# Kernel optimization log

Measured on AMD Instinct MI355X. Metric: run time of the kernel, lower is better.

Reference implementation:

```python
import jax, jax.numpy as jnp
import numpy as np

B, L, D, H = 4, 2048, 256, 512


def silu_backward(x):
    s = jax.nn.silu(x)
    return s + jax.nn.sigmoid(x) * (1.0 - s)


def setup_inputs() -> dict:
    key = jax.random.key(0)
    ks = jax.random.split(key, 12)
    sc = 0.02
    return {
        "x": jax.random.normal(ks[0], (B, L, D), jnp.float32),
        "W1": jax.random.normal(ks[1], (B, H, D), jnp.float32) * sc,
        "W2": jax.random.normal(ks[2], (B, D, H), jnp.float32) * sc,
        "Wq": jax.random.normal(ks[3], (D, D), jnp.float32) * sc,
        "bq": jnp.zeros((D,), jnp.float32),
        "Wk": jax.random.normal(ks[4], (D, D), jnp.float32) * sc,
        "bk": jnp.zeros((D,), jnp.float32),
        "Wv": jax.random.normal(ks[5], (D, D), jnp.float32) * sc,
        "bv": jnp.zeros((D,), jnp.float32),
        "w_lr": jax.random.normal(ks[6], (D,), jnp.float32) * sc,
        "b_lr": jnp.zeros((), jnp.float32),
        "w_wd": jax.random.normal(ks[7], (D,), jnp.float32) * sc,
        "b_wd": jnp.zeros((), jnp.float32),
        "log_base_lr": jnp.asarray(np.log(0.1), jnp.float32),
        "log_base_wd": jnp.asarray(np.log(0.5), jnp.float32),
    }


def reference(x, W1, W2, Wq, bq, Wk, bk, Wv, bv, w_lr, b_lr, w_wd, b_wd, log_base_lr, log_base_wd):
    b, l, d = x.shape
    query = x @ Wq + bq
    key = x @ Wk + bk
    value = x @ Wv + bv
    lr = jnp.exp(log_base_lr) * jax.nn.sigmoid(x @ w_lr + b_lr)          # [b,l]
    log_wd = jnp.log(1.0 - jnp.exp(log_base_wd) * jax.nn.sigmoid(x @ w_wd + b_wd))  # [b,l]

    wd_cross = jnp.exp(jnp.cumsum(log_wd, axis=1))                       # [b,l]
    idx = jnp.arange(l)
    strict_upper = idx[:, None] < idx[None, :]                           # (m, j): j > m
    A = jnp.where(strict_upper[None], log_wd[:, None, :], 0.0)           # [b,m,j]
    wd_inner = jnp.exp(jnp.cumsum(A, axis=2)) * (idx[:, None] <= idx[None, :])[None]  # [b,m,j]

    X1 = key
    Z1 = jnp.einsum('bhd,bld->blh', W1, X1)
    X2 = jax.nn.silu(Z1)
    Z2 = jnp.einsum('bdh,blh->bld', W2, X2)
    grad_Z2 = Z2 - value
    grad_X2 = jnp.einsum('bdh,bld->blh', W2, grad_Z2)
    grad_Z1 = silu_backward(Z1) * grad_X2

    X1_ = query
    mask_X1X1_ = jnp.einsum('bld,bmd->blm', X1, X1_) * wd_inner
    Z1_inner = -jnp.einsum('blh,bl,blm->bmh', grad_Z1, lr, mask_X1X1_)
    Z1_cross = jnp.einsum('bhd,bld,bl->blh', W1, X1_, wd_cross)
    Z1_ = Z1_inner + Z1_cross

    W1_next = (-jnp.einsum('blh,bl,bld->bhd', grad_Z1, lr * wd_inner[:, :, -1], X1)
               + W1 * wd_cross[:, -1][:, None, None])

    X2_ = jax.nn.silu(Z1_)
    mask_X2X2_ = jnp.einsum('blh,bmh->blm', X2, X2_) * wd_inner
    Z2_inner = -jnp.einsum('bld,bl,blm->bmd', grad_Z2, lr, mask_X2X2_)
    Z2_cross = jnp.einsum('bdh,blh,bl->bld', W2, X2_, wd_cross)
    Z2_ = Z2_inner + Z2_cross

    W2_next = (-jnp.einsum('bld,bl,blh->bdh', grad_Z2, lr * wd_inner[:, :, -1], X2)
               + W2 * wd_cross[:, -1][:, None, None])

    return (Z2_, W1_next, W2_next)
```

## Files before the change

kernel.cpp:

```cpp
#include <hip/hip_runtime.h>

typedef __bf16 bf16;
typedef __bf16 bf16x8 __attribute__((ext_vector_type(8)));
typedef __bf16 bf16x4 __attribute__((ext_vector_type(4)));
typedef float  f32x4  __attribute__((ext_vector_type(4)));

#define SB 72
#define CUTOFF -18.0

__device__ __forceinline__ float silu_f(float x){
  float s = 1.f/(1.f+__expf(-x));
  return x*s;
}
__device__ __forceinline__ float silu_bwd_f(float x){
  float s = 1.f/(1.f+__expf(-x));
  float si = x*s;
  return si + s*(1.f-si);
}

struct MArgs {
  const bf16* A; const bf16* B;
  long sA, sB;
  int lda, ldb;
  int M, N, K;
  int mode;
  float* Cf; long sCf;
  bf16*  Cb; long sCb;
  bf16*  Cb2; long sCb2;
  bf16*  Ct;  long sCt;  int ldct;
  int ldc;
  const float* auxf; int ldax; long sAuxf;
  const bf16*  auxb; long sAuxb;
  const float* rowv; long sRowv;
  const double* cd;  long sCd;
  const float* ks;   long sKs;
  const float* clp;  long sClp;
  bf16* Q; bf16* Ko; float* Vo; const float* bqkv;
};

template<int TM>
__device__ __forceinline__ void gemm_body(const MArgs& g, int bm, int bn, int bz)
{
  const int row0 = bm*TM, col0 = bn*64;
  constexpr int NI  = TM/32;
  constexpr int TPR = 256/TM;
  constexpr int EPR = 64/TPR;
  constexpr int NCH = EPR/8;

  const bf16* A = g.A + (long)bz*g.sA;
  const bf16* B = g.B + (long)bz*g.sB;
  const float* ksp = g.ks ? g.ks + (long)bz*g.sKs : (const float*)0;
  const double* cd = g.cd ? g.cd + (long)bz*g.sCd : (const double*)0;
  float* Cf = g.Cf ? g.Cf + (long)bz*g.sCf : (float*)0;
  bf16* Cb  = g.Cb ? g.Cb + (long)bz*g.sCb : (bf16*)0;
  bf16* Cb2 = g.Cb2 ? g.Cb2 + (long)bz*g.sCb2 : (bf16*)0;
  bf16* Ct  = g.Ct ? g.Ct + (long)bz*g.sCt : (bf16*)0;
  const float* auxf = g.auxf ? g.auxf + (long)bz*g.sAuxf : (const float*)0;
  const bf16*  auxb = g.auxb ? g.auxb + (long)bz*g.sAuxb : (const bf16*)0;
  const float* rowv = g.rowv ? g.rowv + (long)bz*g.sRowv : (const float*)0;

  const int tid = threadIdx.x;
  const int mode = g.mode;
  const int lane = tid & 63;
  const int w = tid >> 6;
  const int wr = (w >> 1) * (TM/2), wc = (w & 1) * 32;
  const int l15 = lane & 15;
  const int quad = lane >> 4;

  __shared__ __align__(16) bf16 As[TM*SB];
  __shared__ __align__(16) bf16 Bs[64*SB];

  f32x4 acc[NI][2];
  #pragma unroll
  for (int i=0;i<NI;i++)
    #pragma unroll
    for (int j=0;j<2;j++)
      #pragma unroll
      for (int r=0;r<4;r++) acc[i][j][r] = 0.f;

  const int rowA = tid / TPR, kA = (tid % TPR) * EPR;
  const int rowB = tid >> 2,  kB = (tid & 3) * 16;

  int klo = 0;
  if (cd && ksp) {
    const double cref = cd[g.K-1];
    while (klo + 64 < g.K && (cref - cd[klo+63]) < CUTOFF) klo += 64;
  }

  for (int k0 = klo; k0 < g.K; k0 += 64) {
    {
      const bf16* s = A + (long)(row0+rowA)*g.lda + k0 + kA;
      bf16x8 v[NCH];
      #pragma unroll
      for (int p=0;p<NCH;p++) v[p] = *(const bf16x8*)(s + p*8);
      if (ksp) {
        #pragma unroll
        for (int p=0;p<NCH;p++)
          #pragma unroll
          for (int i=0;i<8;i++)
            v[p][i] = (bf16)((float)v[p][i] * ksp[k0+kA+p*8+i]);
      }
      #pragma unroll
      for (int p=0;p<NCH;p++) *(bf16x8*)&As[rowA*SB + kA + p*8] = v[p];
    }
    {
      const bf16* s = B + (long)(col0+rowB)*g.ldb + k0 + kB;
      *(bf16x8*)&Bs[rowB*SB + kB]     = *(const bf16x8*)s;
      *(bf16x8*)&Bs[rowB*SB + kB + 8] = *(const bf16x8*)(s+8);
    }
    __syncthreads();
    #pragma unroll
    for (int ch=0; ch<2; ch++){
      bf16x8 af[NI], bf2[2];
      #pragma unroll
      for (int i=0;i<NI;i++) af[i]  = *(const bf16x8*)&As[(wr + i*16 + l15)*SB + ch*32 + quad*8];
      #pragma unroll
      for (int j=0;j<2;j++) bf2[j] = *(const bf16x8*)&Bs[(wc + j*16 + l15)*SB + ch*32 + quad*8];
      #pragma unroll
      for (int i=0;i<NI;i++)
        #pragma unroll
        for (int j=0;j<2;j++)
          acc[i][j] = __builtin_amdgcn_mfma_f32_16x16x32_bf16(af[i], bf2[j], acc[i][j], 0, 0, 0);
    }
    __syncthreads();
  }

  float clv = 0.f;
  if (mode == 10) clv = *(g.clp + (long)bz*g.sClp);

  #pragma unroll
  for (int i=0;i<NI;i++){
    const int rb = row0 + wr + i*16 + quad*4;
    #pragma unroll
    for (int j=0;j<2;j++){
      const int c = col0 + wc + j*16 + l15;
      bf16 tv[4]; bool doT = false;
      #pragma unroll
      for (int reg=0; reg<4; reg++){
        const int r = rb + reg;
        float v = acc[i][j][reg];
        const long co = (long)r*g.ldc + c;
        switch (mode) {
          case 1: {
            Cb[co]  = (bf16)v;
            bf16 sv = (bf16)silu_f(v);
            Cb2[co] = sv;
            tv[reg] = sv; doT = true;
          } break;
          case 2: {
            bf16 o = (bf16)(v - auxf[(long)r*g.ldax + c]);
            Cb[co] = o; tv[reg] = o; doT = true;
          } break;
          case 3: {
            bf16 o = (bf16)(silu_bwd_f((float)auxb[(long)r*g.ldax + c]) * v * rowv[r]);
            Cb[co] = o; tv[reg] = o; doT = true;
          } break;
          case 10: {
            Cf[co] = v + auxf[(long)r*g.ldax + c]*clv;
          } break;
          case 11: {
            float o = v + g.bqkv[c];
            if (c < 256)      g.Q [(long)r*256 + c]       = (bf16)o;
            else if (c < 512) { g.Ko[(long)r*256 + (c-256)] = (bf16)o; tv[reg] = (bf16)o; doT = true; }
            else              g.Vo[(long)r*256 + (c-512)] = o;
          } break;
        }
      }
      if (doT && Ct) {
        bf16x4 t4 = { tv[0], tv[1], tv[2], tv[3] };
        if (mode == 11) {
          const int b = rb / g.ldct, l = rb % g.ldct;
          *(bf16x4*)&Ct[(long)b*g.sCt + (long)(c-256)*g.ldct + l] = t4;
        } else {
          *(bf16x4*)&Ct[(long)c*g.ldct + rb] = t4;
        }
      }
    }
  }
}

__global__ __launch_bounds__(256)
void mfma_gemm128(MArgs g){ gemm_body<128>(g, blockIdx.x, blockIdx.y, blockIdx.z); }

__global__ __launch_bounds__(256)
void mfma_gemm64(MArgs g){ gemm_body<64>(g, blockIdx.x, blockIdx.y, blockIdx.z); }

__global__ __launch_bounds__(256)
void wnext_gemm(MArgs g1, MArgs g2){
  const int z = blockIdx.z;
  const MArgs& g = (z < 4) ? g1 : g2;
  const int bz = z & 3;
  if ((int)blockIdx.x*128 >= g.M || (int)blockIdx.y*64 >= g.N) return;
  gemm_body<128>(g, blockIdx.x, blockIdx.y, bz);
}

struct PArgs {
  const bf16 *A, *B1;
  long sA, sB1;
  const double* cd; long sCd;
  const float* lrv; long sLr;
  bf16* P;
};

template<int KS64, int ISLR>
__global__ __launch_bounds__(256)
void pgen(PArgs g)
{
  const int mt = blockIdx.x, slot = blockIdx.y, bz = blockIdx.z;
  const int m0 = mt*64;
  const int l0 = (m0 & ~127) - slot*128;
  if (l0 < 0) return;
  const double* cd = g.cd + (long)bz*g.sCd;
  const int lref = (l0+127 < m0) ? (l0+127) : m0;
  if (cd[m0] - cd[lref] < CUTOFF) return;

  const int K1 = KS64*64;
  const bf16* A  = g.A  + (long)bz*g.sA;
  const bf16* B1 = g.B1 + (long)bz*g.sB1;
  const float* lrv = ISLR ? (g.lrv + (long)bz*g.sLr) : (const float*)0;

  const int tid = threadIdx.x;
  const int lane = tid & 63, w = tid >> 6;
  const int wr = (w>>1)*32, wc = (w&1)*64;
  const int l15 = lane & 15, quad = lane >> 4;
  const int rowA = tid >> 2, kA = (tid & 3) * 16;
  const int rowB = tid >> 1, kB = (tid & 1) * 32;

  __shared__ __align__(16) bf16 As[64*SB];
  __shared__ __align__(16) bf16 Bs[128*SB];

  f32x4 O[2][4];
  #pragma unroll
  for (int i=0;i<2;i++)
    #pragma unroll
    for (int j=0;j<4;j++)
      #pragma unroll
      for (int r=0;r<4;r++) O[i][j][r] = 0.f;

  for (int ks=0; ks<KS64; ks++){
    const int k0 = ks*64;
    {
      const bf16* s = A + (long)(m0+rowA)*K1 + k0 + kA;
      *(bf16x8*)&As[rowA*SB + kA]     = *(const bf16x8*)s;
      *(bf16x8*)&As[rowA*SB + kA + 8] = *(const bf16x8*)(s+8);
    }
    {
      const bf16* s = B1 + (long)(l0+rowB)*K1 + k0 + kB;
      #pragma unroll
      for (int p=0;p<4;p++) *(bf16x8*)&Bs[rowB*SB + kB + p*8] = *(const bf16x8*)(s + p*8);
    }
    __syncthreads();
    #pragma unroll
    for (int ch=0; ch<2; ch++){
      bf16x8 af[2], bfr[4];
      #pragma unroll
      for (int i=0;i<2;i++) af[i]  = *(const bf16x8*)&As[(wr + i*16 + l15)*SB + ch*32 + quad*8];
      #pragma unroll
      for (int j=0;j<4;j++) bfr[j] = *(const bf16x8*)&Bs[(wc + j*16 + l15)*SB + ch*32 + quad*8];
      #pragma unroll
      for (int i=0;i<2;i++)
        #pragma unroll
        for (int j=0;j<4;j++)
          O[i][j] = __builtin_amdgcn_mfma_f32_16x16x32_bf16(af[i], bfr[j], O[i][j], 0, 0, 0);
    }
    __syncthreads();
  }

  bf16* Pt = g.P + (((long)bz*32 + mt)*3 + slot) * (64*128);
  float cl[4], lv[4];
  #pragma unroll
  for (int j=0;j<4;j++){
    const int l = l0 + wc + j*16 + l15;
    cl[j] = (float)cd[l];
    if (ISLR) lv[j] = lrv[l];
  }
  #pragma unroll
  for (int i=0;i<2;i++)
    #pragma unroll
    for (int reg=0; reg<4; reg++){
      const int mloc = wr + i*16 + quad*4 + reg;
      const int m = m0 + mloc;
      const float cm = (float)cd[m];
      #pragma unroll
      for (int j=0;j<4;j++){
        const int lloc = wc + j*16 + l15;
        const int l = l0 + lloc;
        float v = -O[i][j][reg] * __expf(cm - cl[j]);
        if (ISLR) v *= lv[j];
        if (l > m) v = 0.f;
        Pt[mloc*128 + lloc] = (bf16)v;
      }
    }
}

struct CArgs {
  const bf16 *A, *W, *P, *B2;
  long sA, sW, sB2;
  int ldb2;
  const double* cd; long sCd;
  const float* wdc; long sWdc;
  float* Cf; long sCf;
  bf16* Cb; long sCb;
  int ldc;
};

template<int KS64, int SILU, int ZSPLIT>
__global__ __launch_bounds__(256)
void cons(CArgs g)
{
  const int mt = blockIdx.x;
  const int m0 = mt*64, n0 = blockIdx.y*64;
  const int bz   = ZSPLIT ? (blockIdx.z >> 1) : blockIdx.z;
  const int half = ZSPLIT ? (blockIdx.z & 1)  : 0;
  const int K1 = KS64*64;
  const bf16* A  = g.A  + (long)bz*g.sA;
  const bf16* W  = g.W  + (long)bz*g.sW;
  const bf16* B2 = g.B2 + (long)bz*g.sB2;
  const double* cd = g.cd + (long)bz*g.sCd;
  const float* wdc = g.wdc + (long)bz*g.sWdc;

  const int tid = threadIdx.x;
  const int lane = tid & 63, w = tid >> 6;
  const int wr = (w>>1)*32, wc = (w&1)*32;
  const int l15 = lane & 15, quad = lane >> 4;
  const int rowA = tid >> 2, kA = (tid & 3) * 16;

  bool alive[3];
  int nalive = 0;
  #pragma unroll
  for (int s=0;s<3;s++){
    const int l0 = (m0 & ~127) - s*128;
    bool a = (l0 >= 0);
    if (a) {
      const int lref = (l0+127 < m0) ? (l0+127) : m0;
      a = (cd[m0] - cd[lref] >= CUTOFF);
    }
    alive[s] = a; nalive += a ? 1 : 0;
  }
  if (ZSPLIT && half == 1 && nalive == 0) return;

  __shared__ __align__(16) bf16 As[64*SB];
  __shared__ __align__(16) bf16 Bs[64*SB];

  f32x4 O[2][2];
  #pragma unroll
  for (int i=0;i<2;i++)
    #pragma unroll
    for (int j=0;j<2;j++)
      #pragma unroll
      for (int r=0;r<4;r++) O[i][j][r] = 0.f;

  if (half == 0) {
    for (int ks=0; ks<KS64; ks++){
      const int k0 = ks*64;
      {
        const bf16* s = A + (long)(m0+rowA)*K1 + k0 + kA;
        *(bf16x8*)&As[rowA*SB + kA]     = *(const bf16x8*)s;
        *(bf16x8*)&As[rowA*SB + kA + 8] = *(const bf16x8*)(s+8);
      }
      {
        const bf16* s = W + (long)(n0+rowA)*K1 + k0 + kA;
        *(bf16x8*)&Bs[rowA*SB + kA]     = *(const bf16x8*)s;
        *(bf16x8*)&Bs[rowA*SB + kA + 8] = *(const bf16x8*)(s+8);
      }
      __syncthreads();
      #pragma unroll
      for (int ch=0; ch<2; ch++){
        bf16x8 af[2], bfr[2];
        #pragma unroll
        for (int i=0;i<2;i++) af[i]  = *(const bf16x8*)&As[(wr + i*16 + l15)*SB + ch*32 + quad*8];
        #pragma unroll
        for (int j=0;j<2;j++) bfr[j] = *(const bf16x8*)&Bs[(wc + j*16 + l15)*SB + ch*32 + quad*8];
        #pragma unroll
        for (int i=0;i<2;i++)
          #pragma unroll
          for (int j=0;j<2;j++)
            O[i][j] = __builtin_amdgcn_mfma_f32_16x16x32_bf16(af[i], bfr[j], O[i][j], 0, 0, 0);
      }
      __syncthreads();
    }
    #pragma unroll
    for (int i=0;i<2;i++)
      #pragma unroll
      for (int reg=0; reg<4; reg++){
        const float s = wdc[m0 + wr + i*16 + quad*4 + reg];
        #pragma unroll
        for (int j=0;j<2;j++) O[i][j][reg] *= s;
      }
  }

  if (!ZSPLIT || half == 1) {
    for (int s=0; s<3; s++){
      if (!alive[s]) continue;
      const int l0 = (m0 & ~127) - s*128;
      const bf16* Pt = g.P + (((long)bz*32 + mt)*3 + s) * (64*128);
      for (int hk=0; hk<2; hk++){
        {
          const bf16* sp = Pt + (long)rowA*128 + hk*64 + kA;
          *(bf16x8*)&As[rowA*SB + kA]     = *(const bf16x8*)sp;
          *(bf16x8*)&As[rowA*SB + kA + 8] = *(const bf16x8*)(sp+8);
        }
        {
          const bf16* sp = B2 + (long)(n0+rowA)*g.ldb2 + l0 + hk*64 + kA;
          *(bf16x8*)&Bs[rowA*SB + kA]     = *(const bf16x8*)sp;
          *(bf16x8*)&Bs[rowA*SB + kA + 8] = *(const bf16x8*)(sp+8);
        }
        __syncthreads();
        #pragma unroll
        for (int ch=0; ch<2; ch++){
          bf16x8 af[2], bfr[2];
          #pragma unroll
          for (int i=0;i<2;i++) af[i]  = *(const bf16x8*)&As[(wr + i*16 + l15)*SB + ch*32 + quad*8];
          #pragma unroll
          for (int j=0;j<2;j++) bfr[j] = *(const bf16x8*)&Bs[(wc + j*16 + l15)*SB + ch*32 + quad*8];
          #pragma unroll
          for (int i=0;i<2;i++)
            #pragma unroll
            for (int j=0;j<2;j++)
              O[i][j] = __builtin_amdgcn_mfma_f32_16x16x32_bf16(af[i], bfr[j], O[i][j], 0, 0, 0);
        }
        __syncthreads();
      }
    }
  }

  #pragma unroll
  for (int i=0;i<2;i++){
    const int rb = m0 + wr + i*16 + quad*4;
    #pragma unroll
    for (int j=0;j<2;j++){
      const int c = n0 + wc + j*16 + l15;
      #pragma unroll
      for (int reg=0; reg<4; reg++){
        const long co = (long)(rb+reg)*g.ldc + c;
        if (ZSPLIT)     unsafeAtomicAdd(&g.Cf[(long)bz*g.sCf + co], O[i][j][reg]);
        else if (SILU)  g.Cb[(long)bz*g.sCb + co] = (bf16)silu_f(O[i][j][reg]);
        else            g.Cf[(long)bz*g.sCf + co] = O[i][j][reg];
      }
    }
  }
}

struct FrontArgs {
  const float *x, *W1, *W2, *Wq, *Wk, *Wv;
  bf16 *xb, *W1b, *W2b, *Wqkvt, *W2t;
  float* out0;
  const float *wlr, *blr, *wwd, *bwd, *lbl, *lbw;
  float *lr, *lw;
  long LD4, HD4, HD;
};

__global__ __launch_bounds__(256)
void front_kernel(FrontArgs f)
{
  __shared__ bf16 t[64][72];
  const int bid = blockIdx.x;
  const int tid = threadIdx.x;

  if (bid < 1536) {
    const float* src; bf16* dst; long n; long base;
    if (bid < 1024)      { src = f.x;  dst = f.xb;  n = f.LD4; base = (long)bid*2048; }
    else if (bid < 1280) { src = f.W1; dst = f.W1b; n = f.HD4; base = (long)(bid-1024)*2048; }
    else                 { src = f.W2; dst = f.W2b; n = f.HD4; base = (long)(bid-1280)*2048; }
    long i = base + (long)tid*8;
    if (i >= n) return;
    float4 a = *(const float4*)&src[i];
    float4 b = *(const float4*)&src[i+4];
    bf16x8 o;
    o[0]=(bf16)a.x; o[1]=(bf16)a.y; o[2]=(bf16)a.z; o[3]=(bf16)a.w;
    o[4]=(bf16)b.x; o[5]=(bf16)b.y; o[6]=(bf16)b.z; o[7]=(bf16)b.w;
    *(bf16x8*)&dst[i] = o;
    return;
  }
  if (bid < 2560) {
    long i = (long)(bid-1536)*2048 + (long)tid*8;
    float4 z = {0.f,0.f,0.f,0.f};
    *(float4*)&f.out0[i]   = z;
    *(float4*)&f.out0[i+4] = z;
    return;
  }
  if (bid < 2736) {
    const float* ip; bf16* op; int R, C; int r0, c0;
    if (bid < 2608) {
      const int r = bid - 2560;
      const int z = r >> 4, rem = r & 15;
      ip = z==0 ? f.Wq : (z==1 ? f.Wk : f.Wv);
      op = f.Wqkvt + (long)z*256*256;
      R = 256; C = 256;
      r0 = (rem & 3)*64; c0 = (rem >> 2)*64;
    } else {
      const int r = bid - 2608;
      const int b = r >> 5, rem = r & 31;
      ip = f.W2 + (long)b*f.HD;
      op = f.W2t + (long)b*f.HD;
      R = 256; C = 512;
      r0 = (rem & 3)*64; c0 = (rem >> 2)*64;
    }
    const int lr_ = tid>>2, lc = (tid&3)*16;
    #pragma unroll
    for (int q=0;q<4;q++){
      float4 a = *(const float4*)&ip[(long)(r0+lr_)*C + c0+lc + q*4];
      t[lr_][lc+q*4+0] = (bf16)a.x; t[lr_][lc+q*4+1] = (bf16)a.y;
      t[lr_][lc+q*4+2] = (bf16)a.z; t[lr_][lc+q*4+3] = (bf16)a.w;
    }
    __syncthreads();
    const int oc = tid>>2, orr = (tid&3)*16;
    bf16x8 u, v;
    #pragma unroll
    for (int i=0;i<8;i++){ u[i] = t[orr+i][oc]; v[i] = t[orr+8+i][oc]; }
    *(bf16x8*)&op[(long)(c0+oc)*R + r0+orr]   = u;
    *(bf16x8*)&op[(long)(c0+oc)*R + r0+orr+8] = v;
    return;
  }
  {
    const int row  = (bid-2736)*4 + (tid >> 6);
    const int lane = tid & 63;
    const float4 a = ((const float4*)(f.x + (long)row*256))[lane];
    const float4 u = ((const float4*)f.wlr)[lane];
    const float4 w = ((const float4*)f.wwd)[lane];
    float d1 = a.x*u.x + a.y*u.y + a.z*u.z + a.w*u.w;
    float d2 = a.x*w.x + a.y*w.y + a.z*w.z + a.w*w.w;
    #pragma unroll
    for (int off=32; off; off>>=1) {
      d1 += __shfl_down(d1, off);
      d2 += __shfl_down(d2, off);
    }
    if (lane == 0) {
      float s1 = 1.f/(1.f+expf(-(d1 + f.blr[0])));
      f.lr[row] = expf(f.lbl[0]) * s1;
      float s2 = 1.f/(1.f+expf(-(d2 + f.bwd[0])));
      f.lw[row] = logf(1.f - expf(f.lbw[0]) * s2);
    }
  }
}

__global__ __launch_bounds__(256)
void cumsum_kernel(const float* __restrict__ lw, const float* __restrict__ lr,
                   double* __restrict__ cd, float* __restrict__ wdc,
                   float* __restrict__ se1, float* __restrict__ se2, int L,
                   const float* __restrict__ bq, const float* __restrict__ bk,
                   const float* __restrict__ bv, float* __restrict__ bqkv)
{
  const int b = blockIdx.x;
  const int t = threadIdx.x;
  if (b == 4) {
    for (int i = t; i < 768; i += 256)
      bqkv[i] = (i<256) ? bq[i] : ((i<512) ? bk[i-256] : bv[i-512]);
    return;
  }
  const float* lwb = lw + (long)b*L;
  __shared__ double sum_s[256];
  double loc[8];
  double s = 0.0;
  #pragma unroll
  for (int i=0;i<8;i++){ s += (double)lwb[t*8+i]; loc[i] = s; }
  sum_s[t] = s;
  __syncthreads();
  for (int off=1; off<256; off<<=1){
    double v = 0.0;
    if (t >= off) v = sum_s[t-off];
    __syncthreads();
    sum_s[t] += v;
    __syncthreads();
  }
  const double prefix = (t > 0) ? sum_s[t-1] : 0.0;
  const double total  = sum_s[255];
  #pragma unroll
  for (int i=0;i<8;i++){
    double c = prefix + loc[i];
    long idx = (long)b*L + t*8 + i;
    cd[idx]  = c;
    wdc[idx] = (float)exp(c);
    double e = exp(total - c);
    se1[idx] = (float)(-e);
    se2[idx] = (float)(-e) * lr[idx];
  }
}

extern "C" void kernel_launch(void* const* d_in, const int* in_sizes, int n_in,
                              void* d_out, int out_size, void* d_ws, size_t ws_size,
                              hipStream_t stream)
{
  const int Bn = 4, L = 2048, D = 256, H = 512;
  const long LD = (long)L*D, LH = (long)L*H, HD = (long)H*D;

  const float* x   = (const float*)d_in[0];
  const float* W1  = (const float*)d_in[1];
  const float* W2  = (const float*)d_in[2];
  const float* Wq  = (const float*)d_in[3];
  const float* bq  = (const float*)d_in[4];
  const float* Wk  = (const float*)d_in[5];
  const float* bk  = (const float*)d_in[6];
  const float* Wv  = (const float*)d_in[7];
  const float* bv  = (const float*)d_in[8];
  const float* wlr = (const float*)d_in[9];
  const float* blr = (const float*)d_in[10];
  const float* wwd = (const float*)d_in[11];
  const float* bwd = (const float*)d_in[12];
  const float* lbl = (const float*)d_in[13];
  const float* lbw = (const float*)d_in[14];
  (void)in_sizes; (void)n_in; (void)out_size; (void)ws_size;

  float* out0 = (float*)d_out;
  float* out1 = out0 + (long)Bn*LD;
  float* out2 = out1 + (long)Bn*HD;

  char* wsp = (char*)d_ws;
  size_t off = 0;
  auto alloc = [&](size_t bytes)->void*{
    void* p = wsp + off; off += (bytes + 255) & ~(size_t)255; return p;
  };
  bf16* xb    = (bf16*)alloc((size_t)Bn*LD*2);
  bf16* Wqkvt = (bf16*)alloc((size_t)3*D*D*2);
  float* bqkv = (float*)alloc((size_t)3*D*4);
  bf16* W1b  = (bf16*)alloc((size_t)Bn*HD*2);
  bf16* W2b  = (bf16*)alloc((size_t)Bn*HD*2);
  bf16* W2t  = (bf16*)alloc((size_t)Bn*HD*2);
  bf16* Qb   = (bf16*)alloc((size_t)Bn*LD*2);
  bf16* Kb   = (bf16*)alloc((size_t)Bn*LD*2);
  bf16* Kt   = (bf16*)alloc((size_t)Bn*LD*2);
  float* Vf  = (float*)alloc((size_t)Bn*LD*4);
  bf16* Z1b  = (bf16*)alloc((size_t)Bn*LH*2);
  bf16* X2b  = (bf16*)alloc((size_t)Bn*LH*2);
  bf16* X2t  = (bf16*)alloc((size_t)Bn*LH*2);
  bf16* gZb  = (bf16*)alloc((size_t)Bn*LD*2);
  bf16* gZt  = (bf16*)alloc((size_t)Bn*LD*2);
  bf16* A1b  = (bf16*)alloc((size_t)Bn*LH*2);
  bf16* A1t  = (bf16*)alloc((size_t)Bn*LH*2);
  bf16* X2_b = (bf16*)alloc((size_t)Bn*LH*2);
  bf16* Pb1  = (bf16*)alloc((size_t)Bn*32*3*64*128*2);
  bf16* Pb2  = (bf16*)alloc((size_t)Bn*32*3*64*128*2);
  float* lrb = (float*)alloc((size_t)Bn*L*4);
  float* lwb = (float*)alloc((size_t)Bn*L*4);
  float* wdc = (float*)alloc((size_t)Bn*L*4);
  float* se1 = (float*)alloc((size_t)Bn*L*4);
  float* se2 = (float*)alloc((size_t)Bn*L*4);
  double* cdb = (double*)alloc((size_t)Bn*L*8);

  auto run128 = [&](const MArgs& g, int Z){
    dim3 grid(g.M/128, g.N/64, Z);
    mfma_gemm128<<<grid, 256, 0, stream>>>(g);
  };
  auto run64 = [&](const MArgs& g, int Z){
    dim3 grid(g.M/64, g.N/64, Z);
    mfma_gemm64<<<grid, 256, 0, stream>>>(g);
  };

  {
    FrontArgs f{};
    f.x = x; f.W1 = W1; f.W2 = W2; f.Wq = Wq; f.Wk = Wk; f.Wv = Wv;
    f.xb = xb; f.W1b = W1b; f.W2b = W2b; f.Wqkvt = Wqkvt; f.W2t = W2t;
    f.out0 = out0;
    f.wlr = wlr; f.blr = blr; f.wwd = wwd; f.bwd = bwd; f.lbl = lbl; f.lbw = lbw;
    f.lr = lrb; f.lw = lwb;
    f.LD4 = Bn*LD; f.HD4 = Bn*HD; f.HD = HD;
    front_kernel<<<dim3(4784), 256, 0, stream>>>(f);
  }
  cumsum_kernel<<<dim3(5), 256, 0, stream>>>(lwb, lrb, cdb, wdc, se1, se2, L, bq, bk, bv, bqkv);

  {
    MArgs g{}; g.A = xb; g.lda = D; g.B = Wqkvt; g.ldb = D;
    g.M = Bn*L; g.N = 3*D; g.K = D; g.mode = 11; g.ldc = 0;
    g.Q = Qb; g.Ko = Kb; g.Vo = Vf; g.bqkv = bqkv;
    g.Ct = Kt; g.sCt = LD; g.ldct = L;
    run128(g, 1);
  }
  {
    MArgs g{}; g.A = Kb; g.lda = D; g.sA = LD; g.B = W1b; g.ldb = D; g.sB = HD;
    g.M = L; g.N = H; g.K = D; g.mode = 1; g.ldc = H;
    g.Cb = Z1b; g.sCb = LH; g.Cb2 = X2b; g.sCb2 = LH;
    g.Ct = X2t; g.sCt = LH; g.ldct = L; run64(g, Bn);
  }
  {
    MArgs g{}; g.A = X2b; g.lda = H; g.sA = LH; g.B = W2b; g.ldb = H; g.sB = HD;
    g.M = L; g.N = D; g.K = H; g.mode = 2; g.ldc = D;
    g.auxf = Vf; g.ldax = D; g.sAuxf = LD; g.Cb = gZb; g.sCb = LD;
    g.Ct = gZt; g.sCt = LD; g.ldct = L; run64(g, Bn);
  }
  {
    MArgs g{}; g.A = gZb; g.lda = D; g.sA = LD; g.B = W2t; g.ldb = D; g.sB = HD;
    g.M = L; g.N = H; g.K = D; g.mode = 3; g.ldc = H;
    g.auxb = Z1b; g.ldax = H; g.sAuxb = LH; g.rowv = lrb; g.sRowv = L;
    g.Cb = A1b; g.sCb = LH;
    g.Ct = A1t; g.sCt = LH; g.ldct = L; run64(g, Bn);
  }
  {
    PArgs p{};
    p.A = Qb; p.sA = LD; p.B1 = Kb; p.sB1 = LD;
    p.cd = cdb; p.sCd = L; p.P = Pb1;
    pgen<4,0><<<dim3(32,3,Bn), 256, 0, stream>>>(p);
  }
  {
    CArgs c{};
    c.A = Qb; c.sA = LD; c.W = W1b; c.sW = HD;
    c.P = Pb1; c.B2 = A1t; c.sB2 = LH; c.ldb2 = L;
    c.cd = cdb; c.sCd = L; c.wdc = wdc; c.sWdc = L;
    c.Cb = X2_b; c.sCb = LH; c.ldc = H;
    cons<4,1,0><<<dim3(32, H/64, Bn), 256, 0, stream>>>(c);
  }
  {
    PArgs p{};
    p.A = X2_b; p.sA = LH; p.B1 = X2b; p.sB1 = LH;
    p.cd = cdb; p.sCd = L; p.lrv = lrb; p.sLr = L; p.P = Pb2;
    pgen<8,1><<<dim3(32,3,Bn), 256, 0, stream>>>(p);
  }
  {
    CArgs c{};
    c.A = X2_b; c.sA = LH; c.W = W2b; c.sW = HD;
    c.P = Pb2; c.B2 = gZt; c.sB2 = LD; c.ldb2 = L;
    c.cd = cdb; c.sCd = L; c.wdc = wdc; c.sWdc = L;
    c.Cf = out0; c.sCf = LD; c.ldc = D;
    cons<8,0,1><<<dim3(32, D/64, Bn*2), 256, 0, stream>>>(c);
  }
  {
    MArgs g1{}; g1.A = A1t; g1.lda = L; g1.sA = LH; g1.B = Kt; g1.ldb = L; g1.sB = LD;
    g1.M = H; g1.N = D; g1.K = L; g1.mode = 10; g1.ldc = D;
    g1.ks = se1; g1.sKs = L; g1.cd = cdb; g1.sCd = L;
    g1.auxf = W1; g1.ldax = D; g1.sAuxf = HD; g1.clp = wdc + (L-1); g1.sClp = L;
    g1.Cf = out1; g1.sCf = HD;

    MArgs g2{}; g2.A = gZt; g2.lda = L; g2.sA = LD; g2.B = X2t; g2.ldb = L; g2.sB = LH;
    g2.M = D; g2.N = H; g2.K = L; g2.mode = 10; g2.ldc = H;
    g2.ks = se2; g2.sKs = L; g2.cd = cdb; g2.sCd = L;
    g2.auxf = W2; g2.ldax = H; g2.sAuxf = HD; g2.clp = wdc + (L-1); g2.sClp = L;
    g2.Cf = out2; g2.sCf = HD;

    wnext_gemm<<<dim3(4,8,8), 256, 0, stream>>>(g1, g2);
  }
}
```

Measured before the change: 235.3 us.

## Merge independent stages into combined heterogeneous launches and fold decay scales into epilogues

Several independent kernels now share launches through block-index dispatch: QKV GEMM with the cumsum, Z1 GEMM with the first P generation, the A1 GEMM with the W2-next GEMM, and the second P generation with the cross-term consumer and the W1-next GEMM. The per-k decay scaling that used to be applied while loading A tiles in the W-next GEMMs is moved into producer epilogues, which write pre-scaled transposed copies (X2t scaled by se2, and a new A1s buffer scaled by se1). The zero-fill of out0 is dropped; the consumer is split into a cross pass that stores directly and a band pass that adds atomically afterwards. This reduces launch count and tail idle time and removes a per-element multiply from the GEMM main loop, at the cost of larger shared-memory footprints per block, an extra bf16 rounding, and the ordering dependency that the band atomics run after the cross stores.

```diff
diff --git a/kernel.cpp b/kernel.cpp
--- a/kernel.cpp
+++ b/kernel.cpp
@@ -28,18 +28,20 @@
   bf16*  Cb; long sCb;
   bf16*  Cb2; long sCb2;
   bf16*  Ct;  long sCt;  int ldct;
+  bf16*  Ct2; long sCt2;
   int ldc;
   const float* auxf; int ldax; long sAuxf;
   const bf16*  auxb; long sAuxb;
   const float* rowv; long sRowv;
+  const float* rowv2; long sRowv2;
   const double* cd;  long sCd;
-  const float* ks;   long sKs;
   const float* clp;  long sClp;
   bf16* Q; bf16* Ko; float* Vo; const float* bqkv;
 };
 
 template<int TM>
-__device__ __forceinline__ void gemm_body(const MArgs& g, int bm, int bn, int bz)
+__device__ __forceinline__ void gemm_body(const MArgs& g, int bm, int bn, int bz,
+                                          bf16* As, bf16* Bs)
 {
   const int row0 = bm*TM, col0 = bn*64;
   constexpr int NI  = TM/32;
@@ -49,15 +51,16 @@
 
   const bf16* A = g.A + (long)bz*g.sA;
   const bf16* B = g.B + (long)bz*g.sB;
-  const float* ksp = g.ks ? g.ks + (long)bz*g.sKs : (const float*)0;
   const double* cd = g.cd ? g.cd + (long)bz*g.sCd : (const double*)0;
   float* Cf = g.Cf ? g.Cf + (long)bz*g.sCf : (float*)0;
   bf16* Cb  = g.Cb ? g.Cb + (long)bz*g.sCb : (bf16*)0;
   bf16* Cb2 = g.Cb2 ? g.Cb2 + (long)bz*g.sCb2 : (bf16*)0;
   bf16* Ct  = g.Ct ? g.Ct + (long)bz*g.sCt : (bf16*)0;
+  bf16* Ct2 = g.Ct2 ? g.Ct2 + (long)bz*g.sCt2 : (bf16*)0;
   const float* auxf = g.auxf ? g.auxf + (long)bz*g.sAuxf : (const float*)0;
   const bf16*  auxb = g.auxb ? g.auxb + (long)bz*g.sAuxb : (const bf16*)0;
   const float* rowv = g.rowv ? g.rowv + (long)bz*g.sRowv : (const float*)0;
+  const float* rowv2 = g.rowv2 ? g.rowv2 + (long)bz*g.sRowv2 : (const float*)0;
 
   const int tid = threadIdx.x;
   const int mode = g.mode;
@@ -67,9 +70,6 @@
   const int l15 = lane & 15;
   const int quad = lane >> 4;
 
-  __shared__ __align__(16) bf16 As[TM*SB];
-  __shared__ __align__(16) bf16 Bs[64*SB];
-
   f32x4 acc[NI][2];
   #pragma unroll
   for (int i=0;i<NI;i++)
@@ -82,7 +82,7 @@
   const int rowB = tid >> 2,  kB = (tid & 3) * 16;
 
   int klo = 0;
-  if (cd && ksp) {
+  if (cd) {
     const double cref = cd[g.K-1];
     while (klo + 64 < g.K && (cref - cd[klo+63]) < CUTOFF) klo += 64;
   }
@@ -90,18 +90,9 @@
   for (int k0 = klo; k0 < g.K; k0 += 64) {
     {
       const bf16* s = A + (long)(row0+rowA)*g.lda + k0 + kA;
-      bf16x8 v[NCH];
-      #pragma unroll
-      for (int p=0;p<NCH;p++) v[p] = *(const bf16x8*)(s + p*8);
-      if (ksp) {
-        #pragma unroll
-        for (int p=0;p<NCH;p++)
-          #pragma unroll
-          for (int i=0;i<8;i++)
-            v[p][i] = (bf16)((float)v[p][i] * ksp[k0+kA+p*8+i]);
-      }
-      #pragma unroll
-      for (int p=0;p<NCH;p++) *(bf16x8*)&As[rowA*SB + kA + p*8] = v[p];
+      #pragma unroll
+      for (int p=0;p<NCH;p++)
+        *(bf16x8*)&As[rowA*SB + kA + p*8] = *(const bf16x8*)(s + p*8);
     }
     {
       const bf16* s = B + (long)(col0+rowB)*g.ldb + k0 + kB;
@@ -134,7 +125,7 @@
     #pragma unroll
     for (int j=0;j<2;j++){
       const int c = col0 + wc + j*16 + l15;
-      bf16 tv[4]; bool doT = false;
+      bf16 tv[4], tv2[4]; bool doT = false, doT2 = false;
       #pragma unroll
       for (int reg=0; reg<4; reg++){
         const int r = rb + reg;
@@ -143,17 +134,19 @@
         switch (mode) {
           case 1: {
             Cb[co]  = (bf16)v;
-            bf16 sv = (bf16)silu_f(v);
-            Cb2[co] = sv;
-            tv[reg] = sv; doT = true;
+            float sv = silu_f(v);
+            Cb2[co] = (bf16)sv;
+            tv[reg] = (bf16)(sv * rowv[r]); doT = true;
           } break;
           case 2: {
             bf16 o = (bf16)(v - auxf[(long)r*g.ldax + c]);
             Cb[co] = o; tv[reg] = o; doT = true;
           } break;
           case 3: {
-            bf16 o = (bf16)(silu_bwd_f((float)auxb[(long)r*g.ldax + c]) * v * rowv[r]);
-            Cb[co] = o; tv[reg] = o; doT = true;
+            float v3 = silu_bwd_f((float)auxb[(long)r*g.ldax + c]) * v * rowv[r];
+            tv[reg]  = (bf16)v3;
+            tv2[reg] = (bf16)(v3 * rowv2[r]);
+            doT = true; doT2 = true;
           } break;
           case 10: {
             Cf[co] = v + auxf[(long)r*g.ldax + c]*clv;
@@ -175,23 +168,12 @@
           *(bf16x4*)&Ct[(long)c*g.ldct + rb] = t4;
         }
       }
-    }
-  }
-}
-
-__global__ __launch_bounds__(256)
-void mfma_gemm128(MArgs g){ gemm_body<128>(g, blockIdx.x, blockIdx.y, blockIdx.z); }
-
-__global__ __launch_bounds__(256)
-void mfma_gemm64(MArgs g){ gemm_body<64>(g, blockIdx.x, blockIdx.y, blockIdx.z); }
-
-__global__ __launch_bounds__(256)
-void wnext_gemm(MArgs g1, MArgs g2){
-  const int z = blockIdx.z;
-  const MArgs& g = (z < 4) ? g1 : g2;
-  const int bz = z & 3;
-  if ((int)blockIdx.x*128 >= g.M || (int)blockIdx.y*64 >= g.N) return;
-  gemm_body<128>(g, blockIdx.x, blockIdx.y, bz);
+      if (doT2 && Ct2) {
+        bf16x4 t4 = { tv2[0], tv2[1], tv2[2], tv2[3] };
+        *(bf16x4*)&Ct2[(long)c*g.ldct + rb] = t4;
+      }
+    }
+  }
 }
 
 struct PArgs {
@@ -203,10 +185,9 @@
 };
 
 template<int KS64, int ISLR>
-__global__ __launch_bounds__(256)
-void pgen(PArgs g)
-{
-  const int mt = blockIdx.x, slot = blockIdx.y, bz = blockIdx.z;
+__device__ __forceinline__ void pgen_body(const PArgs& g, int mt, int slot, int bz,
+                                          bf16* As, bf16* Bs)
+{
   const int m0 = mt*64;
   const int l0 = (m0 & ~127) - slot*128;
   if (l0 < 0) return;
@@ -225,9 +206,6 @@
   const int l15 = lane & 15, quad = lane >> 4;
   const int rowA = tid >> 2, kA = (tid & 3) * 16;
   const int rowB = tid >> 1, kB = (tid & 1) * 32;
-
-  __shared__ __align__(16) bf16 As[64*SB];
-  __shared__ __align__(16) bf16 Bs[128*SB];
 
   f32x4 O[2][4];
   #pragma unroll
@@ -304,18 +282,14 @@
   int ldc;
 };
 
-template<int KS64, int SILU, int ZSPLIT>
-__global__ __launch_bounds__(256)
-void cons(CArgs g)
-{
-  const int mt = blockIdx.x;
-  const int m0 = mt*64, n0 = blockIdx.y*64;
-  const int bz   = ZSPLIT ? (blockIdx.z >> 1) : blockIdx.z;
-  const int half = ZSPLIT ? (blockIdx.z & 1)  : 0;
+template<int KS64, int SILU, int CROSS, int BAND, int ATOM>
+__device__ __forceinline__ void cons_body(const CArgs& g, int mt, int ny, int bz,
+                                          bf16* As, bf16* Bs)
+{
+  const int m0 = mt*64, n0 = ny*64;
   const int K1 = KS64*64;
   const bf16* A  = g.A  + (long)bz*g.sA;
   const bf16* W  = g.W  + (long)bz*g.sW;
-  const bf16* B2 = g.B2 + (long)bz*g.sB2;
   const double* cd = g.cd + (long)bz*g.sCd;
   const float* wdc = g.wdc + (long)bz*g.sWdc;
 
@@ -327,20 +301,19 @@
 
   bool alive[3];
   int nalive = 0;
-  #pragma unroll
-  for (int s=0;s<3;s++){
-    const int l0 = (m0 & ~127) - s*128;
-    bool a = (l0 >= 0);
-    if (a) {
-      const int lref = (l0+127 < m0) ? (l0+127) : m0;
-      a = (cd[m0] - cd[lref] >= CUTOFF);
-    }
-    alive[s] = a; nalive += a ? 1 : 0;
-  }
-  if (ZSPLIT && half == 1 && nalive == 0) return;
-
-  __shared__ __align__(16) bf16 As[64*SB];
-  __shared__ __align__(16) bf16 Bs[64*SB];
+  if (BAND) {
+    #pragma unroll
+    for (int s=0;s<3;s++){
+      const int l0 = (m0 & ~127) - s*128;
+      bool a = (l0 >= 0);
+      if (a) {
+        const int lref = (l0+127 < m0) ? (l0+127) : m0;
+        a = (cd[m0] - cd[lref] >= CUTOFF);
+      }
+      alive[s] = a; nalive += a ? 1 : 0;
+    }
+    if (!CROSS && nalive == 0) return;
+  }
 
   f32x4 O[2][2];
   #pragma unroll
@@ -350,7 +323,7 @@
       #pragma unroll
       for (int r=0;r<4;r++) O[i][j][r] = 0.f;
 
-  if (half == 0) {
+  if (CROSS) {
     for (int ks=0; ks<KS64; ks++){
       const int k0 = ks*64;
       {
@@ -389,7 +362,8 @@
       }
   }
 
-  if (!ZSPLIT || half == 1) {
+  if (BAND) {
+    const bf16* B2 = g.B2 + (long)bz*g.sB2;
     for (int s=0; s<3; s++){
       if (!alive[s]) continue;
       const int l0 = (m0 & ~127) - s*128;
@@ -433,20 +407,140 @@
       #pragma unroll
       for (int reg=0; reg<4; reg++){
         const long co = (long)(rb+reg)*g.ldc + c;
-        if (ZSPLIT)     unsafeAtomicAdd(&g.Cf[(long)bz*g.sCf + co], O[i][j][reg]);
+        if (ATOM)       unsafeAtomicAdd(&g.Cf[(long)bz*g.sCf + co], O[i][j][reg]);
         else if (SILU)  g.Cb[(long)bz*g.sCb + co] = (bf16)silu_f(O[i][j][reg]);
         else            g.Cf[(long)bz*g.sCf + co] = O[i][j][reg];
       }
     }
   }
+}
+
+struct CumArgs {
+  const float* lw; const float* lr;
+  double* cd; float* wdc; float* se1; float* se2; int L;
+};
+
+__device__ __forceinline__ void cumsum_body(const CumArgs& a, int b)
+{
+  const int t = threadIdx.x;
+  const int L = a.L;
+  const float* lwb = a.lw + (long)b*L;
+  __shared__ double sum_s[256];
+  double loc[8];
+  double s = 0.0;
+  #pragma unroll
+  for (int i=0;i<8;i++){ s += (double)lwb[t*8+i]; loc[i] = s; }
+  sum_s[t] = s;
+  __syncthreads();
+  for (int off=1; off<256; off<<=1){
+    double v = 0.0;
+    if (t >= off) v = sum_s[t-off];
+    __syncthreads();
+    sum_s[t] += v;
+    __syncthreads();
+  }
+  const double prefix = (t > 0) ? sum_s[t-1] : 0.0;
+  const double total  = sum_s[255];
+  #pragma unroll
+  for (int i=0;i<8;i++){
+    double c = prefix + loc[i];
+    long idx = (long)b*L + t*8 + i;
+    a.cd[idx]  = c;
+    a.wdc[idx] = (float)exp(c);
+    double e = exp(total - c);
+    a.se1[idx] = (float)(-e);
+    a.se2[idx] = (float)(-e) * a.lr[idx];
+  }
+}
+
+
+__global__ __launch_bounds__(256)
+void qkv_cum(MArgs g, CumArgs c)
+{
+  __shared__ __align__(16) bf16 sh[192*SB];
+  if (blockIdx.x == 64) {
+    if (blockIdx.y < 4) cumsum_body(c, blockIdx.y);
+    return;
+  }
+  gemm_body<128>(g, blockIdx.x, blockIdx.y, 0, sh, sh + 128*SB);
+}
+
+__global__ __launch_bounds__(256)
+void z1_p1(MArgs g, PArgs p)
+{
+  __shared__ __align__(16) bf16 sh[192*SB];
+  const int bid = blockIdx.x;
+  if (bid < 384) {
+    const int mt = bid & 31, j = bid >> 5;
+    pgen_body<4,0>(p, mt, j % 3, j / 3, sh, sh + 64*SB);
+    return;
+  }
+  const int i = bid - 384;
+  gemm_body<64>(g, i & 31, (i >> 5) & 7, i >> 8, sh, sh + 64*SB);
+}
+
+__global__ __launch_bounds__(256)
+void mfma_gemm64(MArgs g)
+{
+  __shared__ __align__(16) bf16 sh[128*SB];
+  gemm_body<64>(g, blockIdx.x, blockIdx.y, blockIdx.z, sh, sh + 64*SB);
+}
+
+__global__ __launch_bounds__(256)
+void a1_w2n(MArgs ga, MArgs g2)
+{
+  __shared__ __align__(16) bf16 sh[192*SB];
+  const int bid = blockIdx.x;
+  if (bid < 64) {
+    const int bz = bid >> 4, rem = bid & 15;
+    gemm_body<128>(g2, rem >> 3, rem & 7, bz, sh, sh + 128*SB);
+    return;
+  }
+  const int i = bid - 64;
+  gemm_body<64>(ga, i & 31, (i >> 5) & 7, i >> 8, sh, sh + 64*SB);
+}
+
+__global__ __launch_bounds__(256)
+void cons1_k(CArgs c)
+{
+  __shared__ __align__(16) bf16 sh[128*SB];
+  cons_body<4,1,1,1,0>(c, blockIdx.x, blockIdx.y, blockIdx.z, sh, sh + 64*SB);
+}
+
+__global__ __launch_bounds__(256)
+void p2cxw1(PArgs p, CArgs c, MArgs g1)
+{
+  __shared__ __align__(16) bf16 sh[192*SB];
+  const int bid = blockIdx.x;
+  if (bid < 64) {
+    const int bz = bid >> 4, rem = bid & 15;
+    gemm_body<128>(g1, rem & 3, rem >> 2, bz, sh, sh + 128*SB);
+    return;
+  }
+  if (bid < 448) {
+    const int i = bid - 64;
+    const int mt = i & 31, j = i >> 5;
+    pgen_body<8,1>(p, mt, j % 3, j / 3, sh, sh + 64*SB);
+    return;
+  }
+  const int i = bid - 448;
+  cons_body<8,0,1,0,0>(c, i & 31, (i >> 5) & 3, i >> 7, sh, sh + 64*SB);
+}
+
+__global__ __launch_bounds__(256)
+void band_k(CArgs c)
+{
+  __shared__ __align__(16) bf16 sh[128*SB];
+  const int bid = blockIdx.x;
+  cons_body<8,0,0,1,1>(c, bid & 31, (bid >> 5) & 3, bid >> 7, sh, sh + 64*SB);
 }
 
 struct FrontArgs {
   const float *x, *W1, *W2, *Wq, *Wk, *Wv;
   bf16 *xb, *W1b, *W2b, *Wqkvt, *W2t;
-  float* out0;
   const float *wlr, *blr, *wwd, *bwd, *lbl, *lbw;
   float *lr, *lw;
+  const float *bq, *bk, *bv; float* bqkv;
   long LD4, HD4, HD;
 };
 
@@ -472,24 +566,17 @@
     *(bf16x8*)&dst[i] = o;
     return;
   }
-  if (bid < 2560) {
-    long i = (long)(bid-1536)*2048 + (long)tid*8;
-    float4 z = {0.f,0.f,0.f,0.f};
-    *(float4*)&f.out0[i]   = z;
-    *(float4*)&f.out0[i+4] = z;
-    return;
-  }
-  if (bid < 2736) {
+  if (bid < 1712) {
     const float* ip; bf16* op; int R, C; int r0, c0;
-    if (bid < 2608) {
-      const int r = bid - 2560;
+    if (bid < 1584) {
+      const int r = bid - 1536;
       const int z = r >> 4, rem = r & 15;
       ip = z==0 ? f.Wq : (z==1 ? f.Wk : f.Wv);
       op = f.Wqkvt + (long)z*256*256;
       R = 256; C = 256;
       r0 = (rem & 3)*64; c0 = (rem >> 2)*64;
     } else {
-      const int r = bid - 2608;
+      const int r = bid - 1584;
       const int b = r >> 5, rem = r & 31;
       ip = f.W2 + (long)b*f.HD;
       op = f.W2t + (long)b*f.HD;
@@ -512,8 +599,8 @@
     *(bf16x8*)&op[(long)(c0+oc)*R + r0+orr+8] = v;
     return;
   }
-  {
-    const int row  = (bid-2736)*4 + (tid >> 6);
+  if (bid < 3760) {
+    const int row  = (bid-1712)*4 + (tid >> 6);
     const int lane = tid & 63;
     const float4 a = ((const float4*)(f.x + (long)row*256))[lane];
     const float4 u = ((const float4*)f.wlr)[lane];
@@ -531,50 +618,10 @@
       float s2 = 1.f/(1.f+expf(-(d2 + f.bwd[0])));
       f.lw[row] = logf(1.f - expf(f.lbw[0]) * s2);
     }
-  }
-}
-
-__global__ __launch_bounds__(256)
-void cumsum_kernel(const float* __restrict__ lw, const float* __restrict__ lr,
-                   double* __restrict__ cd, float* __restrict__ wdc,
-                   float* __restrict__ se1, float* __restrict__ se2, int L,
-                   const float* __restrict__ bq, const float* __restrict__ bk,
-                   const float* __restrict__ bv, float* __restrict__ bqkv)
-{
-  const int b = blockIdx.x;
-  const int t = threadIdx.x;
-  if (b == 4) {
-    for (int i = t; i < 768; i += 256)
-      bqkv[i] = (i<256) ? bq[i] : ((i<512) ? bk[i-256] : bv[i-512]);
     return;
   }
-  const float* lwb = lw + (long)b*L;
-  __shared__ double sum_s[256];
-  double loc[8];
-  double s = 0.0;
-  #pragma unroll
-  for (int i=0;i<8;i++){ s += (double)lwb[t*8+i]; loc[i] = s; }
-  sum_s[t] = s;
-  __syncthreads();
-  for (int off=1; off<256; off<<=1){
-    double v = 0.0;
-    if (t >= off) v = sum_s[t-off];
-    __syncthreads();
-    sum_s[t] += v;
-    __syncthreads();
-  }
-  const double prefix = (t > 0) ? sum_s[t-1] : 0.0;
-  const double total  = sum_s[255];
-  #pragma unroll
-  for (int i=0;i<8;i++){
-    double c = prefix + loc[i];
-    long idx = (long)b*L + t*8 + i;
-    cd[idx]  = c;
-    wdc[idx] = (float)exp(c);
-    double e = exp(total - c);
-    se1[idx] = (float)(-e);
-    se2[idx] = (float)(-e) * lr[idx];
-  }
+  for (int i = tid; i < 768; i += 256)
+    f.bqkv[i] = (i<256) ? f.bq[i] : ((i<512) ? f.bk[i-256] : f.bv[i-512]);
 }
 
 extern "C" void kernel_launch(void* const* d_in, const int* in_sizes, int n_in,
@@ -625,8 +672,8 @@
   bf16* X2t  = (bf16*)alloc((size_t)Bn*LH*2);
   bf16* gZb  = (bf16*)alloc((size_t)Bn*LD*2);
   bf16* gZt  = (bf16*)alloc((size_t)Bn*LD*2);
-  bf16* A1b  = (bf16*)alloc((size_t)Bn*LH*2);
   bf16* A1t  = (bf16*)alloc((size_t)Bn*LH*2);
+  bf16* A1s  = (bf16*)alloc((size_t)Bn*LH*2);
   bf16* X2_b = (bf16*)alloc((size_t)Bn*LH*2);
   bf16* Pb1  = (bf16*)alloc((size_t)Bn*32*3*64*128*2);
   bf16* Pb2  = (bf16*)alloc((size_t)Bn*32*3*64*128*2);
@@ -637,58 +684,57 @@
   float* se2 = (float*)alloc((size_t)Bn*L*4);
   double* cdb = (double*)alloc((size_t)Bn*L*8);
 
-  auto run128 = [&](const MArgs& g, int Z){
-    dim3 grid(g.M/128, g.N/64, Z);
-    mfma_gemm128<<<grid, 256, 0, stream>>>(g);
-  };
-  auto run64 = [&](const MArgs& g, int Z){
-    dim3 grid(g.M/64, g.N/64, Z);
-    mfma_gemm64<<<grid, 256, 0, stream>>>(g);
-  };
-
   {
     FrontArgs f{};
     f.x = x; f.W1 = W1; f.W2 = W2; f.Wq = Wq; f.Wk = Wk; f.Wv = Wv;
     f.xb = xb; f.W1b = W1b; f.W2b = W2b; f.Wqkvt = Wqkvt; f.W2t = W2t;
-    f.out0 = out0;
     f.wlr = wlr; f.blr = blr; f.wwd = wwd; f.bwd = bwd; f.lbl = lbl; f.lbw = lbw;
     f.lr = lrb; f.lw = lwb;
+    f.bq = bq; f.bk = bk; f.bv = bv; f.bqkv = bqkv;
     f.LD4 = Bn*LD; f.HD4 = Bn*HD; f.HD = HD;
-    front_kernel<<<dim3(4784), 256, 0, stream>>>(f);
-  }
-  cumsum_kernel<<<dim3(5), 256, 0, stream>>>(lwb, lrb, cdb, wdc, se1, se2, L, bq, bk, bv, bqkv);
-
+    front_kernel<<<dim3(3761), 256, 0, stream>>>(f);
+  }
   {
     MArgs g{}; g.A = xb; g.lda = D; g.B = Wqkvt; g.ldb = D;
     g.M = Bn*L; g.N = 3*D; g.K = D; g.mode = 11; g.ldc = 0;
     g.Q = Qb; g.Ko = Kb; g.Vo = Vf; g.bqkv = bqkv;
     g.Ct = Kt; g.sCt = LD; g.ldct = L;
-    run128(g, 1);
+    CumArgs ca{ lwb, lrb, cdb, wdc, se1, se2, L };
+    qkv_cum<<<dim3(65, 12), 256, 0, stream>>>(g, ca);
   }
   {
     MArgs g{}; g.A = Kb; g.lda = D; g.sA = LD; g.B = W1b; g.ldb = D; g.sB = HD;
     g.M = L; g.N = H; g.K = D; g.mode = 1; g.ldc = H;
     g.Cb = Z1b; g.sCb = LH; g.Cb2 = X2b; g.sCb2 = LH;
-    g.Ct = X2t; g.sCt = LH; g.ldct = L; run64(g, Bn);
+    g.Ct = X2t; g.sCt = LH; g.ldct = L;
+    g.rowv = se2; g.sRowv = L;
+    PArgs p{};
+    p.A = Qb; p.sA = LD; p.B1 = Kb; p.sB1 = LD;
+    p.cd = cdb; p.sCd = L; p.P = Pb1;
+    z1_p1<<<dim3(384 + 1024), 256, 0, stream>>>(g, p);
   }
   {
     MArgs g{}; g.A = X2b; g.lda = H; g.sA = LH; g.B = W2b; g.ldb = H; g.sB = HD;
     g.M = L; g.N = D; g.K = H; g.mode = 2; g.ldc = D;
     g.auxf = Vf; g.ldax = D; g.sAuxf = LD; g.Cb = gZb; g.sCb = LD;
-    g.Ct = gZt; g.sCt = LD; g.ldct = L; run64(g, Bn);
+    g.Ct = gZt; g.sCt = LD; g.ldct = L;
+    mfma_gemm64<<<dim3(32, 4, 4), 256, 0, stream>>>(g);
   }
   {
-    MArgs g{}; g.A = gZb; g.lda = D; g.sA = LD; g.B = W2t; g.ldb = D; g.sB = HD;
-    g.M = L; g.N = H; g.K = D; g.mode = 3; g.ldc = H;
-    g.auxb = Z1b; g.ldax = H; g.sAuxb = LH; g.rowv = lrb; g.sRowv = L;
-    g.Cb = A1b; g.sCb = LH;
-    g.Ct = A1t; g.sCt = LH; g.ldct = L; run64(g, Bn);
-  }
-  {
-    PArgs p{};
-    p.A = Qb; p.sA = LD; p.B1 = Kb; p.sB1 = LD;
-    p.cd = cdb; p.sCd = L; p.P = Pb1;
-    pgen<4,0><<<dim3(32,3,Bn), 256, 0, stream>>>(p);
+    MArgs ga{}; ga.A = gZb; ga.lda = D; ga.sA = LD; ga.B = W2t; ga.ldb = D; ga.sB = HD;
+    ga.M = L; ga.N = H; ga.K = D; ga.mode = 3; ga.ldc = H;
+    ga.auxb = Z1b; ga.ldax = H; ga.sAuxb = LH;
+    ga.rowv = lrb; ga.sRowv = L; ga.rowv2 = se1; ga.sRowv2 = L;
+    ga.Ct = A1t; ga.sCt = LH; ga.ldct = L;
+    ga.Ct2 = A1s; ga.sCt2 = LH;
+
+    MArgs g2{}; g2.A = gZt; g2.lda = L; g2.sA = LD; g2.B = X2t; g2.ldb = L; g2.sB = LH;
+    g2.M = D; g2.N = H; g2.K = L; g2.mode = 10; g2.ldc = H;
+    g2.cd = cdb; g2.sCd = L;
+    g2.auxf = W2; g2.ldax = H; g2.sAuxf = HD; g2.clp = wdc + (L-1); g2.sClp = L;
+    g2.Cf = out2; g2.sCf = HD;
+
+    a1_w2n<<<dim3(64 + 1024), 256, 0, stream>>>(ga, g2);
   }
   {
     CArgs c{};
@@ -696,13 +742,7 @@
     c.P = Pb1; c.B2 = A1t; c.sB2 = LH; c.ldb2 = L;
     c.cd = cdb; c.sCd = L; c.wdc = wdc; c.sWdc = L;
     c.Cb = X2_b; c.sCb = LH; c.ldc = H;
-    cons<4,1,0><<<dim3(32, H/64, Bn), 256, 0, stream>>>(c);
-  }
-  {
-    PArgs p{};
-    p.A = X2_b; p.sA = LH; p.B1 = X2b; p.sB1 = LH;
-    p.cd = cdb; p.sCd = L; p.lrv = lrb; p.sLr = L; p.P = Pb2;
-    pgen<8,1><<<dim3(32,3,Bn), 256, 0, stream>>>(p);
+    cons1_k<<<dim3(32, H/64, Bn), 256, 0, stream>>>(c);
   }
   {
     CArgs c{};
@@ -710,21 +750,18 @@
     c.P = Pb2; c.B2 = gZt; c.sB2 = LD; c.ldb2 = L;
     c.cd = cdb; c.sCd = L; c.wdc = wdc; c.sWdc = L;
     c.Cf = out0; c.sCf = LD; c.ldc = D;
-    cons<8,0,1><<<dim3(32, D/64, Bn*2), 256, 0, stream>>>(c);
-  }
-  {
-    MArgs g1{}; g1.A = A1t; g1.lda = L; g1.sA = LH; g1.B = Kt; g1.ldb = L; g1.sB = LD;
+
+    PArgs p{};
+    p.A = X2_b; p.sA = LH; p.B1 = X2b; p.sB1 = LH;
+    p.cd = cdb; p.sCd = L; p.lrv = lrb; p.sLr = L; p.P = Pb2;
+
+    MArgs g1{}; g1.A = A1s; g1.lda = L; g1.sA = LH; g1.B = Kt; g1.ldb = L; g1.sB = LD;
     g1.M = H; g1.N = D; g1.K = L; g1.mode = 10; g1.ldc = D;
-    g1.ks = se1; g1.sKs = L; g1.cd = cdb; g1.sCd = L;
+    g1.cd = cdb; g1.sCd = L;
     g1.auxf = W1; g1.ldax = D; g1.sAuxf = HD; g1.clp = wdc + (L-1); g1.sClp = L;
     g1.Cf = out1; g1.sCf = HD;
 
-    MArgs g2{}; g2.A = gZt; g2.lda = L; g2.sA = LD; g2.B = X2t; g2.ldb = L; g2.sB = LH;
-    g2.M = D; g2.N = H; g2.K = L; g2.mode = 10; g2.ldc = H;
-    g2.ks = se2; g2.sKs = L; g2.cd = cdb; g2.sCd = L;
-    g2.auxf = W2; g2.ldax = H; g2.sAuxf = HD; g2.clp = wdc + (L-1); g2.sClp = L;
-    g2.Cf = out2; g2.sCf = HD;
-
-    wnext_gemm<<<dim3(4,8,8), 256, 0, stream>>>(g1, g2);
-  }
-}
+    p2cxw1<<<dim3(64 + 384 + 512), 256, 0, stream>>>(p, c, g1);
+    band_k<<<dim3(512), 256, 0, stream>>>(c);
+  }
+}
```

New measurement: 286.6 us. +21.8%, slower.
